# Kernel tuning notes

Measured on AMD Instinct MI355X. Metric: run time of the kernel, lower is better.

Reference implementation:

```python
import jax, jax.numpy as jnp
import numpy as np
import math

B, T, HIDDEN = 1, 2048, 2048
N_HEADS, N_KV = 16, 8
HD = HIDDEN // N_HEADS  # 128
EPS = 1e-6
THETA = 1e6


def _rmsnorm(x, w, eps=EPS):
    return x * jax.lax.rsqrt(jnp.mean(x * x, axis=-1, keepdims=True) + eps) * w


def _rope(x, sin, cos):
    # even/odd split, non-interleaved concat output (matches get_rope)
    x1 = x[..., 0::2]
    x2 = x[..., 1::2]
    s = sin[None, :, None, :]  # [1, T, 1, HD//2]
    c = cos[None, :, None, :]
    return jnp.concatenate([x1 * c - x2 * s, x1 * s + x2 * c], axis=-1)


def setup_inputs() -> dict:
    key = jax.random.key(0)
    ks = jax.random.split(key, 6)
    x = jax.random.normal(ks[0], (B, T, HIDDEN), dtype=jnp.float32)
    Wq = 0.02 * jax.random.normal(ks[1], (HIDDEN, 2 * HIDDEN), dtype=jnp.float32)
    Wk = 0.02 * jax.random.normal(ks[2], (HIDDEN, N_KV * HD), dtype=jnp.float32)
    Wv = 0.02 * jax.random.normal(ks[3], (HIDDEN, N_KV * HD), dtype=jnp.float32)
    Wo = 0.02 * jax.random.normal(ks[4], (2 * HIDDEN, HIDDEN), dtype=jnp.float32)
    q_norm_w = jnp.ones((2 * HD,), dtype=jnp.float32)
    k_norm_w = jnp.ones((HD,), dtype=jnp.float32)
    inv_freq = 1.0 / (THETA ** (jnp.arange(0, HD, 2, dtype=jnp.float32) / HD))
    freqs = jnp.arange(T, dtype=jnp.float32)[:, None] * inv_freq[None, :]  # [T, HD//2]
    return {"x": x, "Wq": Wq, "Wk": Wk, "Wv": Wv, "Wo": Wo,
            "q_norm_w": q_norm_w, "k_norm_w": k_norm_w,
            "sin": jnp.sin(freqs), "cos": jnp.cos(freqs)}


def reference(x, Wq, Wk, Wv, Wo, q_norm_w, k_norm_w, sin, cos):
    b, t, _ = x.shape
    # projections
    q = (x @ Wq).reshape(b, t, N_HEADS, 2 * HD)
    k = (x @ Wk).reshape(b, t, N_KV, HD)
    v = (x @ Wv).reshape(b, t, N_KV, HD)
    # per-head QK RMSNorm (q_norm over 2*head_dim)
    q = _rmsnorm(q, q_norm_w)
    k = _rmsnorm(k, k_norm_w)
    # split q into 2*N_HEADS attention heads of dim HD, apply RoPE
    hq = 2 * N_HEADS
    q = _rope(q.reshape(b, t, hq, HD), sin, cos)
    k = _rope(k, sin, cos)
    # GQA: repeat kv heads
    g = hq // N_KV
    k = jnp.repeat(k, g, axis=2)  # [b, t, hq, HD]
    v = jnp.repeat(v, g, axis=2)
    # attention: no causal mask in the original module
    att = jnp.einsum('bqhd,bkhd->bhqk', q, k) / math.sqrt(HD)
    p = jax.nn.softmax(att, axis=-1)
    out = jnp.einsum('bhqk,bkhd->bqhd', p, v).reshape(b, t, hq * HD)
    return out @ Wo
```

## Files before the change

### kernel.cpp

```cpp
#include <hip/hip_runtime.h>

typedef unsigned short u16;
typedef __attribute__((ext_vector_type(8))) short bf16x8;
typedef __attribute__((ext_vector_type(4))) short s16x4;
typedef __attribute__((ext_vector_type(4))) float f32x4;

__device__ __forceinline__ float bf2f(u16 u) {
  union { unsigned u; float f; } c; c.u = ((unsigned)u) << 16; return c.f;
}
__device__ __forceinline__ u16 f2bf(float f) {
  union { float f; unsigned u; } c; c.f = f;
  return (u16)((c.u + 0x7fffu + ((c.u >> 16) & 1u)) >> 16);
}
#if __has_builtin(__builtin_amdgcn_cvt_pk_bf16_f32)
__device__ __forceinline__ unsigned pkbf(float a, float b) {
  auto v = __builtin_amdgcn_cvt_pk_bf16_f32(a, b);
  return __builtin_bit_cast(unsigned, v);
}
#else
__device__ __forceinline__ unsigned pkbf(float a, float b) {
  return (unsigned)f2bf(a) | ((unsigned)f2bf(b) << 16);
}
#endif
#if __has_builtin(__builtin_amdgcn_mfma_f32_16x16x16bf16_1k)
#define MFMA16(a, b, c) __builtin_amdgcn_mfma_f32_16x16x16bf16_1k(a, b, c, 0, 0, 0)
#define HAVE_MFMA16 1
#endif
#if __has_builtin(__builtin_amdgcn_permlane16_swap) && \
    __has_builtin(__builtin_amdgcn_permlane32_swap)
#define HAVE_PLSWAP 1
__device__ __forceinline__ void plswap32(unsigned& a, unsigned& b) {
  auto r = __builtin_amdgcn_permlane32_swap(a, b, false, false);
  a = r[0]; b = r[1];
}
__device__ __forceinline__ void plswap16(unsigned& a, unsigned& b) {
  auto r = __builtin_amdgcn_permlane16_swap(a, b, false, false);
  a = r[0]; b = r[1];
}
#endif
#if __has_builtin(__builtin_amdgcn_exp2f)
#define EXP2(x) __builtin_amdgcn_exp2f(x)
#else
#define EXP2(x) __expf((x) * 0.69314718f)
#endif
__device__ __forceinline__ void gl2lds16(const u16* g, u16* l) {
  __builtin_amdgcn_global_load_lds(
      (const __attribute__((address_space(1))) void*)g,
      (__attribute__((address_space(3))) void*)l, 16, 0, 0);
}

__device__ __forceinline__ void tr_cast_tile(const float* __restrict__ in,
                                             u16* __restrict__ out,
                                             int ldin, int ldout, int bx, int by) {
  __shared__ u16 tile[64][66];
  const int tx = threadIdx.x;
  const int lr = tx & 31, lc = tx >> 5;
  const int r0 = by << 6, c0 = bx << 6;
#pragma unroll
  for (int i = 0; i < 8; ++i) {
    int r = lc + (i << 3);
    float2 v = *(const float2*)&in[(size_t)(r0 + r) * ldin + c0 + (lr << 1)];
    *(unsigned*)&tile[r][lr << 1] = pkbf(v.x, v.y);
  }
  __syncthreads();
#pragma unroll
  for (int i = 0; i < 8; ++i) {
    int c = lc + (i << 3);
    unsigned v = (unsigned)tile[lr << 1][c] | ((unsigned)tile[(lr << 1) + 1][c] << 16);
    *(unsigned*)&out[(size_t)(c0 + c) * ldout + r0 + (lr << 1)] = v;
  }
}

__global__ __launch_bounds__(256) void prep(const float* __restrict__ x,
                                            u16* __restrict__ xb,
                                            const float* __restrict__ Wq,
                                            u16* __restrict__ WqT,
                                            const float* __restrict__ Wk,
                                            u16* __restrict__ WkT,
                                            const float* __restrict__ Wv,
                                            u16* __restrict__ WvT) {
  int b = blockIdx.x;
  if (b < 2048) {
    int i = (b * 256 + threadIdx.x) * 8;
    float4 a = *(const float4*)&x[i];
    float4 c = *(const float4*)&x[i + 4];
    union { unsigned u[4]; bf16x8 v; } w;
    w.u[0] = pkbf(a.x, a.y); w.u[1] = pkbf(a.z, a.w);
    w.u[2] = pkbf(c.x, c.y); w.u[3] = pkbf(c.z, c.w);
    *(bf16x8*)&xb[i] = w.v;
  } else if (b < 4096) {
    int t = b - 2048;
    tr_cast_tile(Wq, WqT, 4096, 2048, t & 63, t >> 6);
  } else if (b < 4608) {
    int t = b - 4096;
    tr_cast_tile(Wk, WkT, 1024, 2048, t & 15, t >> 4);
  } else {
    int t = b - 4608;
    tr_cast_tile(Wv, WvT, 1024, 2048, t & 15, t >> 4);
  }
}

__global__ __launch_bounds__(256) void transpose_cast(const float* __restrict__ in,
                                                      u16* __restrict__ out,
                                                      int ldin, int ldout) {
  tr_cast_tile(in, out, ldin, ldout, blockIdx.x, blockIdx.y);
}

__global__ __launch_bounds__(256) void gemm_bt(const u16* __restrict__ A,
                                               const u16* __restrict__ BT,
                                               u16* __restrict__ C,
                                               int M, int N, int K) {
  __shared__ u16 Asl[2][128 * 32];
  __shared__ u16 Bsl[2][128 * 32];
  const int tid = threadIdx.x;
  const int lane = tid & 63, wv = tid >> 6;
  const int lr = lane & 15, qd = lane >> 4;
  const int wr = wv >> 1, wc = wv & 1;
  const int m0 = blockIdx.y << 7, n0 = blockIdx.x << 7;
  const int srow = lane >> 2, scol = (lane & 3) << 3;
  const u16* Ag = &A[(size_t)(m0 + wv * 32 + srow) * K + scol];
  const u16* Bg = &BT[(size_t)(n0 + wv * 32 + srow) * K + scol];
  const size_t rstr16 = (size_t)16 * K;
  f32x4 acc[4][4] = {};
  for (int k0 = 0; k0 < K; k0 += 64) {
    __syncthreads();
#pragma unroll
    for (int p = 0; p < 2; ++p) {
#pragma unroll
      for (int hh = 0; hh < 2; ++hh) {
        gl2lds16(Ag + k0 + p * 32 + hh * rstr16, &Asl[p][wv * 1024 + hh * 512]);
        gl2lds16(Bg + k0 + p * 32 + hh * rstr16, &Bsl[p][wv * 1024 + hh * 512]);
      }
    }
    __syncthreads();
#pragma unroll
    for (int p = 0; p < 2; ++p) {
      bf16x8 af[4], bfr[4];
#pragma unroll
      for (int i = 0; i < 4; ++i) {
        af[i]  = *(const bf16x8*)&Asl[p][(wr * 64 + i * 16 + lr) * 32 + qd * 8];
        bfr[i] = *(const bf16x8*)&Bsl[p][(wc * 64 + i * 16 + lr) * 32 + qd * 8];
      }
#pragma unroll
      for (int mi = 0; mi < 4; ++mi)
#pragma unroll
        for (int ni = 0; ni < 4; ++ni)
          acc[mi][ni] = __builtin_amdgcn_mfma_f32_16x16x32_bf16(
              af[mi], bfr[ni], acc[mi][ni], 0, 0, 0);
    }
  }
#pragma unroll
  for (int mi = 0; mi < 4; ++mi)
#pragma unroll
    for (int ni = 0; ni < 4; ++ni)
#pragma unroll
      for (int r = 0; r < 4; ++r)
        C[(size_t)(m0 + wr * 64 + mi * 16 + qd * 4 + r) * N +
          n0 + wc * 64 + ni * 16 + lr] = f2bf(acc[mi][ni][r]);
}

__global__ __launch_bounds__(256) void gemm_bt_sk(const u16* __restrict__ A,
                                                  const u16* __restrict__ BT,
                                                  float* __restrict__ C,
                                                  int M, int N, int K, int kspan) {
  __shared__ u16 Asl[2][128 * 32];
  __shared__ u16 Bsl[2][128 * 32];
  const int tid = threadIdx.x;
  const int lane = tid & 63, wv = tid >> 6;
  const int lr = lane & 15, qd = lane >> 4;
  const int wr = wv >> 1, wc = wv & 1;
  const int m0 = blockIdx.y << 7, n0 = blockIdx.x << 7;
  const int kbeg = blockIdx.z * kspan;
  const int srow = lane >> 2, scol = (lane & 3) << 3;
  const u16* Ag = &A[(size_t)(m0 + wv * 32 + srow) * K + kbeg + scol];
  const u16* Bg = &BT[(size_t)(n0 + wv * 32 + srow) * K + kbeg + scol];
  const size_t rstr16 = (size_t)16 * K;
  f32x4 acc[4][4] = {};
  for (int k0 = 0; k0 < kspan; k0 += 64) {
    __syncthreads();
#pragma unroll
    for (int p = 0; p < 2; ++p) {
#pragma unroll
      for (int hh = 0; hh < 2; ++hh) {
        gl2lds16(Ag + k0 + p * 32 + hh * rstr16, &Asl[p][wv * 1024 + hh * 512]);
        gl2lds16(Bg + k0 + p * 32 + hh * rstr16, &Bsl[p][wv * 1024 + hh * 512]);
      }
    }
    __syncthreads();
#pragma unroll
    for (int p = 0; p < 2; ++p) {
      bf16x8 af[4], bfr[4];
#pragma unroll
      for (int i = 0; i < 4; ++i) {
        af[i]  = *(const bf16x8*)&Asl[p][(wr * 64 + i * 16 + lr) * 32 + qd * 8];
        bfr[i] = *(const bf16x8*)&Bsl[p][(wc * 64 + i * 16 + lr) * 32 + qd * 8];
      }
#pragma unroll
      for (int mi = 0; mi < 4; ++mi)
#pragma unroll
        for (int ni = 0; ni < 4; ++ni)
          acc[mi][ni] = __builtin_amdgcn_mfma_f32_16x16x32_bf16(
              af[mi], bfr[ni], acc[mi][ni], 0, 0, 0);
    }
  }
#pragma unroll
  for (int mi = 0; mi < 4; ++mi)
#pragma unroll
    for (int ni = 0; ni < 4; ++ni)
#pragma unroll
      for (int r = 0; r < 4; ++r)
        unsafeAtomicAdd(&C[(size_t)(m0 + wr * 64 + mi * 16 + qd * 4 + r) * N +
                           n0 + wc * 64 + ni * 16 + lr], acc[mi][ni][r]);
}

__global__ __launch_bounds__(256) void norm_vt(u16* __restrict__ QKV,
                                               u16* __restrict__ VTb,
                                               const float* __restrict__ qw,
                                               const float* __restrict__ kw,
                                               const float* __restrict__ sinb,
                                               const float* __restrict__ cosb) {
  int b = blockIdx.x;
  if (b >= 2048) {
    __shared__ u16 tile[64][66];
    int t = b - 2048;
    const int tx = threadIdx.x;
    const int lr = tx & 31, lc = tx >> 5;
    const int r0 = (t >> 4) << 6, c0 = (t & 15) << 6;
    const u16* in = QKV + 5120;
#pragma unroll
    for (int i = 0; i < 8; ++i) {
      int r = lc + (i << 3);
      unsigned v = *(const unsigned*)&in[(size_t)(r0 + r) * 6144 + c0 + (lr << 1)];
      *(unsigned*)&tile[r][lr << 1] = v;
    }
    __syncthreads();
#pragma unroll
    for (int i = 0; i < 8; ++i) {
      int c = lc + (i << 3);
      unsigned v = (unsigned)tile[lr << 1][c] | ((unsigned)tile[(lr << 1) + 1][c] << 16);
      *(unsigned*)&VTb[(size_t)(c0 + c) * 2048 + r0 + (lr << 1)] = v;
    }
    return;
  }
  const int t = b;
  const int wv = threadIdx.x >> 6, l = threadIdx.x & 63;
  const float sv = sinb[t * 64 + l];
  const float cv = cosb[t * 64 + l];
  const float qscale = 0.12753102543f;
  u16* Q = QKV + (size_t)t * 6144;
  u16* Kb = Q + 4096;
  for (int j = wv; j < 16; j += 4) {
    u16* base = Q + j * 256;
    float x0 = bf2f(base[2 * l]);
    float x1 = bf2f(base[2 * l + 1]);
    float x2 = bf2f(base[128 + 2 * l]);
    float x3 = bf2f(base[129 + 2 * l]);
    float ss = x0 * x0 + x1 * x1 + x2 * x2 + x3 * x3;
#pragma unroll
    for (int m = 1; m < 64; m <<= 1) ss += __shfl_xor(ss, m, 64);
    float rn = rsqrtf(ss * (1.0f / 256.0f) + 1e-6f);
    float w0 = qw[2 * l], w1 = qw[2 * l + 1];
    float w2 = qw[128 + 2 * l], w3 = qw[129 + 2 * l];
    x0 *= rn * w0; x1 *= rn * w1; x2 *= rn * w2; x3 *= rn * w3;
    base[l]       = f2bf((x0 * cv - x1 * sv) * qscale);
    base[64 + l]  = f2bf((x0 * sv + x1 * cv) * qscale);
    base[128 + l] = f2bf((x2 * cv - x3 * sv) * qscale);
    base[192 + l] = f2bf((x2 * sv + x3 * cv) * qscale);
  }
  for (int j = wv; j < 8; j += 4) {
    u16* base = Kb + j * 128;
    float x0 = bf2f(base[2 * l]);
    float x1 = bf2f(base[2 * l + 1]);
    float ss = x0 * x0 + x1 * x1;
#pragma unroll
    for (int m = 1; m < 64; m <<= 1) ss += __shfl_xor(ss, m, 64);
    float rn = rsqrtf(ss * (1.0f / 128.0f) + 1e-6f);
    float w0 = kw[2 * l], w1 = kw[2 * l + 1];
    x0 *= rn * w0; x1 *= rn * w1;
    base[l]      = f2bf(x0 * cv - x1 * sv);
    base[64 + l] = f2bf(x0 * sv + x1 * cv);
  }
}

__global__ __launch_bounds__(256, 2) void flash(const u16* __restrict__ QKV,
                                                const u16* __restrict__ VTb,
                                                u16* __restrict__ O,
                                                float* __restrict__ L) {
  __shared__ u16 Ks0[64 * 128];
  __shared__ u16 Ks1[64 * 128];
  __shared__ u16 Vs0[128 * 64];
  __shared__ u16 Vs1[128 * 64];
  const int tid = threadIdx.x;
  const int wv = tid >> 6, lane = tid & 63;
  const int c = lane & 15, qd = lane >> 4;
  const int wgid = blockIdx.x;
  const int r8 = wgid & 7, t_ = wgid >> 3;
  const int qx = t_ & 15, hh = t_ >> 4;
  const int h = r8 + (hh << 3);
  const int kv = h >> 2;
  const int qb = (qx << 7) + wv * 32;
  const int cx = c & 7;
  const int krow_off = lane >> 4;
  const int kpb = lane & 15;
  const int vrow_off = lane >> 3;
  const int vpb = lane & 7;
  bf16x8 qf[2][4];
#pragma unroll
  for (int ms = 0; ms < 2; ++ms)
#pragma unroll
    for (int ks = 0; ks < 4; ++ks)
      qf[ms][ks] = *(const bf16x8*)&QKV[(size_t)(qb + ms * 16 + c) * 6144 +
                                        h * 128 + ks * 32 + qd * 8];
  f32x4 o[2][8] = {};
  float lrun[2] = {0.f, 0.f};

  auto stage = [&](int k0, u16* Kd, u16* Vd) {
#pragma unroll
    for (int it = 0; it < 4; ++it) {
      int rbase = (wv * 4 + it) * 4;
      int r = rbase + krow_off;
      int klb = kpb ^ (r & 7);
      gl2lds16(&QKV[(size_t)(k0 + r) * 6144 + 4096 + kv * 128 + klb * 8],
               &Kd[rbase * 128]);
      int dbase = (wv * 4 + it) * 8;
      int d = dbase + vrow_off;
      int vlb = vpb ^ (d & 7);
      gl2lds16(&VTb[(size_t)(kv * 128 + d) * 2048 + k0 + vlb * 8],
               &Vd[dbase * 64]);
    }
  };

  auto compute = [&](const u16* Ks, const u16* Vs) {
    f32x4 s[2][4];
    __builtin_amdgcn_s_setprio(1);
#pragma unroll
    for (int ns = 0; ns < 4; ++ns) {
      f32x4 a0 = {0.f, 0.f, 0.f, 0.f}, a1 = {0.f, 0.f, 0.f, 0.f};
#pragma unroll
      for (int ks = 0; ks < 4; ++ks) {
        bf16x8 kf = *(const bf16x8*)
            &Ks[(ns * 16 + c) * 128 + (((4 * ks + qd) ^ cx) << 3)];
        a0 = __builtin_amdgcn_mfma_f32_16x16x32_bf16(kf, qf[0][ks], a0, 0, 0, 0);
        a1 = __builtin_amdgcn_mfma_f32_16x16x32_bf16(kf, qf[1][ks], a1, 0, 0, 0);
      }
      s[0][ns] = a0; s[1][ns] = a1;
    }
    __builtin_amdgcn_s_setprio(0);
#pragma unroll
    for (int ms = 0; ms < 2; ++ms) {
      float rs = 0.f;
#pragma unroll
      for (int ns = 0; ns < 4; ++ns)
#pragma unroll
        for (int r = 0; r < 4; ++r) {
          float p = EXP2(s[ms][ns][r]);
          s[ms][ns][r] = p; rs += p;
        }
      lrun[ms] += rs;
    }
#ifdef HAVE_PLSWAP
#pragma unroll
    for (int t2 = 0; t2 < 2; ++t2) {
      bf16x8 pB[2];
#pragma unroll
      for (int ms = 0; ms < 2; ++ms) {
        unsigned p0 = pkbf(s[ms][2 * t2][0],     s[ms][2 * t2][1]);
        unsigned p1 = pkbf(s[ms][2 * t2][2],     s[ms][2 * t2][3]);
        unsigned p2 = pkbf(s[ms][2 * t2 + 1][0], s[ms][2 * t2 + 1][1]);
        unsigned p3 = pkbf(s[ms][2 * t2 + 1][2], s[ms][2 * t2 + 1][3]);
        plswap32(p0, p2); plswap16(p0, p2);
        plswap32(p1, p3); plswap16(p1, p3);
        union { unsigned u[4]; bf16x8 v; } bb;
        bb.u[0] = p0; bb.u[1] = p1; bb.u[2] = p2; bb.u[3] = p3;
        pB[ms] = bb.v;
      }
      __builtin_amdgcn_s_setprio(1);
#pragma unroll
      for (int n8 = 0; n8 < 8; ++n8) {
        bf16x8 vf = *(const bf16x8*)
            &Vs[(n8 * 16 + c) * 64 + (((4 * t2 + qd) ^ cx) << 3)];
        o[0][n8] = __builtin_amdgcn_mfma_f32_16x16x32_bf16(vf, pB[0], o[0][n8], 0, 0, 0);
        o[1][n8] = __builtin_amdgcn_mfma_f32_16x16x32_bf16(vf, pB[1], o[1][n8], 0, 0, 0);
      }
      __builtin_amdgcn_s_setprio(0);
    }
#elif defined(HAVE_MFMA16)
#pragma unroll
    for (int ns = 0; ns < 4; ++ns) {
      s16x4 pb[2];
#pragma unroll
      for (int ms = 0; ms < 2; ++ms) {
        union { unsigned u[2]; s16x4 v; } pu;
        pu.u[0] = pkbf(s[ms][ns][0], s[ms][ns][1]);
        pu.u[1] = pkbf(s[ms][ns][2], s[ms][ns][3]);
        pb[ms] = pu.v;
      }
      const int voff = ((((2 * ns) + (qd >> 1)) ^ cx) << 3) + (qd & 1) * 4;
#pragma unroll
      for (int n8 = 0; n8 < 8; ++n8) {
        s16x4 vf = *(const s16x4*)&Vs[(n8 * 16 + c) * 64 + voff];
        o[0][n8] = MFMA16(vf, pb[0], o[0][n8]);
        o[1][n8] = MFMA16(vf, pb[1], o[1][n8]);
      }
    }
#else
    unsigned pk[2][4][2];
#pragma unroll
    for (int ms = 0; ms < 2; ++ms)
#pragma unroll
      for (int ns = 0; ns < 4; ++ns) {
        pk[ms][ns][0] = pkbf(s[ms][ns][0], s[ms][ns][1]);
        pk[ms][ns][1] = pkbf(s[ms][ns][2], s[ms][ns][3]);
      }
    const bool hi = lane >= 32;
    const int sl0 = ((lane >> 4) & 1) * 32 + c;
    const int sl1 = sl0 + 16;
#pragma unroll
    for (int t2 = 0; t2 < 2; ++t2) {
      union { int i[4]; bf16x8 v; } pb[2];
#pragma unroll
      for (int ms = 0; ms < 2; ++ms)
#pragma unroll
        for (int dw = 0; dw < 4; ++dw) {
          int rg = dw & 1;
          int sl = dw < 2 ? sl0 : sl1;
          int va = __shfl((int)pk[ms][2 * t2][rg], sl, 64);
          int vb = __shfl((int)pk[ms][2 * t2 + 1][rg], sl, 64);
          pb[ms].i[dw] = hi ? vb : va;
        }
#pragma unroll
      for (int n8 = 0; n8 < 8; ++n8) {
        bf16x8 vf = *(const bf16x8*)
            &Vs[(n8 * 16 + c) * 64 + (((4 * t2 + qd) ^ cx) << 3)];
        o[0][n8] = __builtin_amdgcn_mfma_f32_16x16x32_bf16(vf, pb[0].v, o[0][n8], 0, 0, 0);
        o[1][n8] = __builtin_amdgcn_mfma_f32_16x16x32_bf16(vf, pb[1].v, o[1][n8], 0, 0, 0);
      }
    }
#endif
  };

  stage(0, Ks0, Vs0);
#pragma unroll 1
  for (int k0 = 0; k0 < 2048; k0 += 128) {
    __syncthreads();
    stage(k0 + 64, Ks1, Vs1);
    compute(Ks0, Vs0);
    __syncthreads();
    if (k0 + 128 < 2048) stage(k0 + 128, Ks0, Vs0);
    compute(Ks1, Vs1);
  }
#pragma unroll
  for (int ms = 0; ms < 2; ++ms) {
    lrun[ms] += __shfl_xor(lrun[ms], 16, 64);
    lrun[ms] += __shfl_xor(lrun[ms], 32, 64);
  }
  if (qd == 0) {
    L[(qb + c) * 32 + h] = lrun[0];
    L[(qb + 16 + c) * 32 + h] = lrun[1];
  }
#pragma unroll
  for (int ms = 0; ms < 2; ++ms)
#pragma unroll
    for (int n8 = 0; n8 < 8; ++n8) {
      union { unsigned u[2]; s16x4 v; } w;
      w.u[0] = pkbf(o[ms][n8][0], o[ms][n8][1]);
      w.u[1] = pkbf(o[ms][n8][2], o[ms][n8][3]);
      *(s16x4*)&O[(size_t)(qb + ms * 16 + c) * 4096 + h * 128 + n8 * 16 + qd * 4] = w.v;
    }
}

__global__ __launch_bounds__(256) void combine(u16* __restrict__ O,
                                               const float* __restrict__ L) {
  int i8 = (blockIdx.x * 256 + threadIdx.x) * 8;
  int q = i8 >> 12, h = (i8 >> 7) & 31;
  float inv = 1.0f / L[q * 32 + h];
  bf16x8 a = *(bf16x8*)&O[i8];
  union { unsigned u[4]; bf16x8 v; } w;
#pragma unroll
  for (int j = 0; j < 4; ++j) {
    float e0 = bf2f((u16)a[2 * j]) * inv;
    float e1 = bf2f((u16)a[2 * j + 1]) * inv;
    w.u[j] = pkbf(e0, e1);
  }
  *(bf16x8*)&O[i8] = w.v;
}

extern "C" void kernel_launch(void* const* d_in, const int* in_sizes, int n_in,
                              void* d_out, int out_size, void* d_ws, size_t ws_size,
                              hipStream_t stream) {
  const float* x    = (const float*)d_in[0];
  const float* Wq   = (const float*)d_in[1];
  const float* Wk   = (const float*)d_in[2];
  const float* Wv   = (const float*)d_in[3];
  const float* Wo   = (const float*)d_in[4];
  const float* qnw  = (const float*)d_in[5];
  const float* knw  = (const float*)d_in[6];
  const float* sinb = (const float*)d_in[7];
  const float* cosb = (const float*)d_in[8];
  float* out = (float*)d_out;
  char* ws = (char*)d_ws;
  const size_t MB = 1024 * 1024;
  u16* WqkvT = (u16*)(ws + 0 * MB);
  u16* Op0   = (u16*)(ws + 0 * MB);
  float* L0f = (float*)(ws + 16 * MB);
  u16* QKV = (u16*)(ws + 24 * MB);
  u16* WoT = (u16*)(ws + 24 * MB);
  u16* xb  = (u16*)(ws + 48 * MB);
  u16* VTb = (u16*)(ws + 64 * MB);

  prep<<<5120, 256, 0, stream>>>(x, xb, Wq, WqkvT,
                                 Wk, WqkvT + (size_t)4096 * 2048,
                                 Wv, WqkvT + (size_t)5120 * 2048);
  gemm_bt<<<dim3(48, 16), 256, 0, stream>>>(xb, WqkvT, QKV, 2048, 6144, 2048);
  norm_vt<<<2560, 256, 0, stream>>>(QKV, VTb, qnw, knw, sinb, cosb);
  flash<<<512, 256, 0, stream>>>(QKV, VTb, Op0, L0f);
  transpose_cast<<<dim3(32, 64), 256, 0, stream>>>(Wo, WoT, 2048, 4096);
  combine<<<4096, 256, 0, stream>>>(Op0, L0f);
  hipMemsetAsync(out, 0, (size_t)2048 * 2048 * 4, stream);
  gemm_bt_sk<<<dim3(16, 16, 2), 256, 0, stream>>>(Op0, WoT, out, 2048, 2048, 4096, 2048);
  (void)in_sizes; (void)n_in; (void)out_size; (void)ws_size;
}
```

Baseline: 369.5 us.

## Swizzle GEMM block order and read V directly from global in flash attention

The two GEMM kernels remap block indices with a grouped swizzle so that concurrently running blocks share A/B tiles in L2. The flash kernel stops staging V^T tiles through LDS and loads V fragments straight from global memory inside the PV MFMA loop, halving LDS use per block. This removes LDS writes and bank traffic for V, but exposes global-load latency inside the inner loop and relies on L2 hits across the four heads that share each KV head.

```diff
diff --git a/kernel.cpp b/kernel.cpp
--- a/kernel.cpp
+++ b/kernel.cpp
@@ -116,7 +116,9 @@
   const int lane = tid & 63, wv = tid >> 6;
   const int lr = lane & 15, qd = lane >> 4;
   const int wr = wv >> 1, wc = wv & 1;
-  const int m0 = blockIdx.y << 7, n0 = blockIdx.x << 7;
+  const int id = blockIdx.y * 48 + blockIdx.x;
+  const int swz = (id & 7) * 96 + (id >> 3);
+  const int m0 = (swz / 48) << 7, n0 = (swz % 48) << 7;
   const int srow = lane >> 2, scol = (lane & 3) << 3;
   const u16* Ag = &A[(size_t)(m0 + wv * 32 + srow) * K + scol];
   const u16* Bg = &BT[(size_t)(n0 + wv * 32 + srow) * K + scol];
@@ -169,7 +171,9 @@
   const int lane = tid & 63, wv = tid >> 6;
   const int lr = lane & 15, qd = lane >> 4;
   const int wr = wv >> 1, wc = wv & 1;
-  const int m0 = blockIdx.y << 7, n0 = blockIdx.x << 7;
+  const int id = blockIdx.y * 16 + blockIdx.x;
+  const int swz = (id & 7) * 32 + (id >> 3);
+  const int m0 = (swz >> 4) << 7, n0 = (swz & 15) << 7;
   const int kbeg = blockIdx.z * kspan;
   const int srow = lane >> 2, scol = (lane & 3) << 3;
   const u16* Ag = &A[(size_t)(m0 + wv * 32 + srow) * K + kbeg + scol];
@@ -288,8 +292,6 @@
                                                 float* __restrict__ L) {
   __shared__ u16 Ks0[64 * 128];
   __shared__ u16 Ks1[64 * 128];
-  __shared__ u16 Vs0[128 * 64];
-  __shared__ u16 Vs1[128 * 64];
   const int tid = threadIdx.x;
   const int wv = tid >> 6, lane = tid & 63;
   const int c = lane & 15, qd = lane >> 4;
@@ -302,8 +304,7 @@
   const int cx = c & 7;
   const int krow_off = lane >> 4;
   const int kpb = lane & 15;
-  const int vrow_off = lane >> 3;
-  const int vpb = lane & 7;
+  const u16* Vg = &VTb[(size_t)(kv * 128) * 2048];
   bf16x8 qf[2][4];
 #pragma unroll
   for (int ms = 0; ms < 2; ++ms)
@@ -314,7 +315,7 @@
   f32x4 o[2][8] = {};
   float lrun[2] = {0.f, 0.f};
 
-  auto stage = [&](int k0, u16* Kd, u16* Vd) {
+  auto stage = [&](int k0, u16* Kd) {
 #pragma unroll
     for (int it = 0; it < 4; ++it) {
       int rbase = (wv * 4 + it) * 4;
@@ -322,15 +323,10 @@
       int klb = kpb ^ (r & 7);
       gl2lds16(&QKV[(size_t)(k0 + r) * 6144 + 4096 + kv * 128 + klb * 8],
                &Kd[rbase * 128]);
-      int dbase = (wv * 4 + it) * 8;
-      int d = dbase + vrow_off;
-      int vlb = vpb ^ (d & 7);
-      gl2lds16(&VTb[(size_t)(kv * 128 + d) * 2048 + k0 + vlb * 8],
-               &Vd[dbase * 64]);
     }
   };
 
-  auto compute = [&](const u16* Ks, const u16* Vs) {
+  auto compute = [&](const u16* Ks, int k0v) {
     f32x4 s[2][4];
     __builtin_amdgcn_s_setprio(1);
 #pragma unroll
@@ -378,7 +374,7 @@
 #pragma unroll
       for (int n8 = 0; n8 < 8; ++n8) {
         bf16x8 vf = *(const bf16x8*)
-            &Vs[(n8 * 16 + c) * 64 + (((4 * t2 + qd) ^ cx) << 3)];
+            &Vg[(size_t)(n8 * 16 + c) * 2048 + k0v + (4 * t2 + qd) * 8];
         o[0][n8] = __builtin_amdgcn_mfma_f32_16x16x32_bf16(vf, pB[0], o[0][n8], 0, 0, 0);
         o[1][n8] = __builtin_amdgcn_mfma_f32_16x16x32_bf16(vf, pB[1], o[1][n8], 0, 0, 0);
       }
@@ -395,10 +391,11 @@
         pu.u[1] = pkbf(s[ms][ns][2], s[ms][ns][3]);
         pb[ms] = pu.v;
       }
-      const int voff = ((((2 * ns) + (qd >> 1)) ^ cx) << 3) + (qd & 1) * 4;
 #pragma unroll
       for (int n8 = 0; n8 < 8; ++n8) {
-        s16x4 vf = *(const s16x4*)&Vs[(n8 * 16 + c) * 64 + voff];
+        s16x4 vf = *(const s16x4*)
+            &Vg[(size_t)(n8 * 16 + c) * 2048 + k0v +
+                ((2 * ns) + (qd >> 1)) * 8 + (qd & 1) * 4];
         o[0][n8] = MFMA16(vf, pb[0], o[0][n8]);
         o[1][n8] = MFMA16(vf, pb[1], o[1][n8]);
       }
@@ -431,7 +428,7 @@
 #pragma unroll
       for (int n8 = 0; n8 < 8; ++n8) {
         bf16x8 vf = *(const bf16x8*)
-            &Vs[(n8 * 16 + c) * 64 + (((4 * t2 + qd) ^ cx) << 3)];
+            &Vg[(size_t)(n8 * 16 + c) * 2048 + k0v + (4 * t2 + qd) * 8];
         o[0][n8] = __builtin_amdgcn_mfma_f32_16x16x32_bf16(vf, pb[0].v, o[0][n8], 0, 0, 0);
         o[1][n8] = __builtin_amdgcn_mfma_f32_16x16x32_bf16(vf, pb[1].v, o[1][n8], 0, 0, 0);
       }
@@ -439,15 +436,15 @@
 #endif
   };
 
-  stage(0, Ks0, Vs0);
+  stage(0, Ks0);
 #pragma unroll 1
   for (int k0 = 0; k0 < 2048; k0 += 128) {
     __syncthreads();
-    stage(k0 + 64, Ks1, Vs1);
-    compute(Ks0, Vs0);
-    __syncthreads();
-    if (k0 + 128 < 2048) stage(k0 + 128, Ks0, Vs0);
-    compute(Ks1, Vs1);
+    stage(k0 + 64, Ks1);
+    compute(Ks0, k0);
+    __syncthreads();
+    if (k0 + 128 < 2048) stage(k0 + 128, Ks0);
+    compute(Ks1, k0 + 64);
   }
 #pragma unroll
   for (int ms = 0; ms < 2; ++ms) {
```

After: 435.8 us. +17.9%, slower.
